# Kernel optimization log

Hardware: AMD Instinct MI355X
Metric: run time of the kernel (lower is better)

The kernel has to match this reference:

```python
import jax, jax.numpy as jnp
import numpy as np

B, NCOL, NCOND = 1024, 64, 64
NRODT, D, NEST, NFOREST, NHID, NCLASS = 1024, 4, 128, 100, 128, 10
EPS = 1e-5


def setup_inputs() -> dict:
    key = jax.random.key(0)
    ks = jax.random.split(key, 16)
    rng = np.random.default_rng(0)
    s = 0.1
    inp = {
        'x': jax.random.normal(ks[0], (B, NCOL), jnp.float32),
        # phi_1 numerical grouped conv: groups=NCOL, in_per_g=1, out_per_g=NCOND
        'w1': jax.random.normal(ks[1], (NCOL, 1, NCOND), jnp.float32) * s,
        'b1': jax.random.normal(ks[2], (NCOL * NCOND,), jnp.float32) * s,
        # rODTConstruction fixed permutation of the 4096 conditions
        'perm': jnp.asarray(rng.permutation(NCOND * NCOL), jnp.int32),
        'gn1_g': jnp.ones((NCOND * NCOL,), jnp.float32),
        'gn1_b': jnp.zeros((NCOND * NCOL,), jnp.float32),
        # phi_2 grouped convs: groups=NRODT, block D->D then D->1
        'w2a': jax.random.normal(ks[3], (NRODT, D, D), jnp.float32) * s,
        'b2a': jax.random.normal(ks[4], (NRODT * D,), jnp.float32) * s,
        'gn2_g': jnp.ones((NCOND * NCOL,), jnp.float32),
        'gn2_b': jnp.zeros((NCOND * NCOL,), jnp.float32),
        'w2b': jax.random.normal(ks[5], (NRODT, D, 1), jnp.float32) * s,
        'b2b': jax.random.normal(ks[6], (NRODT,), jnp.float32) * s,
        'E': jax.random.normal(ks[7], (NRODT, NHID), jnp.float32) * s,
        # eval-mode sample_without_replacement buffer: per-forest subset of rODTs
        'swr': jnp.asarray(np.argsort(rng.random((NFOREST, NRODT)), axis=-1)[:, :NEST], jnp.int32),
        'ln1_g': jnp.ones((NHID,), jnp.float32),
        'ln1_b': jnp.zeros((NHID,), jnp.float32),
        'lin1_w': jax.random.normal(ks[8], (NHID, NHID), jnp.float32) * s,
        'lin1_b': jax.random.normal(ks[9], (NHID,), jnp.float32) * s,
        'ln2_g': jnp.ones((NHID,), jnp.float32),
        'ln2_b': jnp.zeros((NHID,), jnp.float32),
        'lin2_w': jax.random.normal(ks[10], (NHID, NCLASS), jnp.float32) * s,
        'lin2_b': jax.random.normal(ks[11], (NCLASS,), jnp.float32) * s,
    }
    return inp


def _group_norm(v, g, gamma, beta):
    # v: (B, C), normalize within each of g channel groups (L=1 in the torch module)
    b, c = v.shape
    vg = v.reshape(b, g, c // g)
    mu = vg.mean(-1, keepdims=True)
    var = vg.var(-1, keepdims=True)
    vn = ((vg - mu) / jnp.sqrt(var + EPS)).reshape(b, c)
    return vn * gamma + beta


def _layer_norm(v, gamma, beta):
    mu = v.mean(-1, keepdims=True)
    var = v.var(-1, keepdims=True)
    return (v - mu) / jnp.sqrt(var + EPS) * gamma + beta


def reference(x, w1, b1, perm, gn1_g, gn1_b, w2a, b2a, gn2_g, gn2_b, w2b, b2b,
              E, swr, ln1_g, ln1_b, lin1_w, lin1_b, ln2_g, ln2_b, lin2_w, lin2_b):
    b = x.shape[0]
    # ConditionGeneration (numerical only): block-diag GEMV with in_per_group=1
    M = jax.nn.sigmoid(x[:, :, None] * w1[None, :, 0, :] + b1.reshape(NCOL, NCOND))  # (B, NCOL, NCOND)
    M = M.transpose(0, 2, 1)  # (B, NCOND, NCOL)
    # rODTConstruction: flatten + fixed permutation
    O = M.reshape(b, NCOND * NCOL)[:, perm]  # (B, 4096)
    # phi_2: GroupNorm -> grouped conv (D->D) -> ReLU -> GroupNorm -> grouped conv (D->1)
    h = _group_norm(O, NRODT, gn1_g, gn1_b).reshape(b, NRODT, D)
    h = jnp.einsum('bgi,gio->bgo', h, w2a) + b2a.reshape(NRODT, D)
    h = jax.nn.relu(h).reshape(b, NRODT * D)
    h = _group_norm(h, NRODT, gn2_g, gn2_b).reshape(b, NRODT, D)
    w = jnp.einsum('bgi,gio->bgo', h, w2b)[..., 0] + b2b  # (B, NRODT), n_head=1
    # forest construction: gather rODT subsets, softmax over estimators, weighted embed sum
    ws = jax.nn.softmax(w[:, swr], axis=-1)  # (B, NFOREST, NEST)
    Es = E[swr]  # (NFOREST, NEST, NHID)
    F = jnp.einsum('bfe,feh->bfh', ws, Es)  # (B, NFOREST, NHID)
    # phi_3 bagging MLP (eval mode: dropout = identity)
    z = _layer_norm(F, ln1_g, ln1_b)
    z = jax.nn.relu(z @ lin1_w + lin1_b)
    z = _layer_norm(z, ln2_g, ln2_b)
    y_hats = z @ lin2_w + lin2_b  # (B, NFOREST, NCLASS)
    return y_hats.mean(1)  # (B, NCLASS)
```

## Files before the change

### kernel.cpp

```cpp
#include <hip/hip_runtime.h>


#define B_      1024
#define NCOL_   64
#define NCOND_  64
#define NRODT_  1024
#define NEST_   128
#define NFOREST_ 100
#define NHID_   128
#define NCLASS_ 10
#define EPS_    1e-5f

typedef __bf16 bf16_t;
typedef bf16_t bf16x8 __attribute__((ext_vector_type(8)));
typedef float  f32x4  __attribute__((ext_vector_type(4)));

#define MFMA16(a,b,c) __builtin_amdgcn_mfma_f32_16x16x32_bf16(a,b,c,0,0,0)

#define EG_FRAGS   (NFOREST_*4*8*64)
#define W1_FRAGS   (4*8*64)
#define L2_FRAGS   (4*64)

__global__ __launch_bounds__(256) void k_prep(
    const float* __restrict__ E,     const int*   __restrict__ swr,
    const float* __restrict__ lin1w, const float* __restrict__ lin2w,
    const float* __restrict__ x,
    bf16_t* __restrict__ Eh,  bf16_t* __restrict__ El,
    bf16_t* __restrict__ Wh,  bf16_t* __restrict__ Wl,
    bf16_t* __restrict__ L2h, bf16_t* __restrict__ L2l,
    float*  __restrict__ x_t, float* __restrict__ accz)
{
    int blk = blockIdx.x, tid = threadIdx.x;
    if (blk < 800) {
        int t = blk * 256 + tid;
        int lane = t & 63, nn = (t >> 6) & 7, kk = (t >> 9) & 3, f = t >> 11;
        int q = lane >> 4, n = nn * 16 + (lane & 15);
        bf16x8 hi, lo;
#pragma unroll
        for (int j = 0; j < 8; ++j) {
            int e = kk * 32 + q * 8 + j;
            int r = swr[f * NEST_ + e];
            float v = E[r * NHID_ + n];
            bf16_t h = (bf16_t)v;
            hi[j] = h; lo[j] = (bf16_t)(v - (float)h);
        }
        *(bf16x8*)(Eh + (size_t)t * 8) = hi;
        *(bf16x8*)(El + (size_t)t * 8) = lo;
    } else if (blk < 808) {
        int t = (blk - 800) * 256 + tid;
        int lane = t & 63, nn = (t >> 6) & 7, kk = t >> 9;
        int q = lane >> 4, n = nn * 16 + (lane & 15);
        bf16x8 hi, lo;
#pragma unroll
        for (int j = 0; j < 8; ++j) {
            int k = kk * 32 + q * 8 + j;
            float v = lin1w[k * NHID_ + n];
            bf16_t h = (bf16_t)v;
            hi[j] = h; lo[j] = (bf16_t)(v - (float)h);
        }
        *(bf16x8*)(Wh + t * 8) = hi;
        *(bf16x8*)(Wl + t * 8) = lo;
    } else if (blk == 808) {
        int t = tid;
        int lane = t & 63, kk = t >> 6;
        int q = lane >> 4, n = lane & 15;
        bf16x8 hi, lo;
#pragma unroll
        for (int j = 0; j < 8; ++j) {
            int k = kk * 32 + q * 8 + j;
            float v = (n < NCLASS_) ? lin2w[k * NCLASS_ + n] : 0.f;
            bf16_t h = (bf16_t)v;
            hi[j] = h; lo[j] = (bf16_t)(v - (float)h);
        }
        *(bf16x8*)(L2h + t * 8) = hi;
        *(bf16x8*)(L2l + t * 8) = lo;
    } else if (blk < 1065) {
        int t = (blk - 809) * 256 + tid;
        x_t[t] = x[(t & 1023) * NCOL_ + (t >> 10)];
    } else {
        int t = (blk - 1065) * 256 + tid;
        if (t < B_ * NCLASS_) accz[t] = 0.f;
    }
}

__global__ __launch_bounds__(256) void k_rodt(
    const float* __restrict__ x_t,  const float* __restrict__ w1,
    const float* __restrict__ b1,   const int*  __restrict__ perm,
    const float* __restrict__ gn1g, const float* __restrict__ gn1b,
    const float* __restrict__ w2a,  const float* __restrict__ b2a,
    const float* __restrict__ gn2g, const float* __restrict__ gn2b,
    const float* __restrict__ w2b,  const float* __restrict__ b2b,
    float* __restrict__ w_t)
{
    int g  = blockIdx.x;
    int bq = threadIdx.x * 4;

    int4 p4 = ((const int4*)perm)[g];
    int col[4]  = { p4.x & 63, p4.y & 63, p4.z & 63, p4.w & 63 };
    int cond[4] = { p4.x >> 6, p4.y >> 6, p4.z >> 6, p4.w >> 6 };
    float w1v[4], b1v[4];
#pragma unroll
    for (int j = 0; j < 4; ++j) {
        w1v[j] = w1[col[j] * NCOND_ + cond[j]];
        b1v[j] = b1[col[j] * NCOND_ + cond[j]];
    }
    float4 g1  = ((const float4*)gn1g)[g];
    float4 o1  = ((const float4*)gn1b)[g];
    float4 ba  = ((const float4*)b2a)[g];
    float4 g2  = ((const float4*)gn2g)[g];
    float4 o2  = ((const float4*)gn2b)[g];
    float4 wb4 = ((const float4*)w2b)[g];
    float  bb  = b2b[g];
    float4 wa[4];
    const float4* w2a4 = (const float4*)w2a;
#pragma unroll
    for (int i = 0; i < 4; ++i) wa[i] = w2a4[g * 4 + i];

    float xv[4][4];
#pragma unroll
    for (int j = 0; j < 4; ++j) {
        float4 t = *(const float4*)&x_t[col[j] * B_ + bq];
        xv[j][0] = t.x; xv[j][1] = t.y; xv[j][2] = t.z; xv[j][3] = t.w;
    }

    float outv[4];
#pragma unroll
    for (int bi = 0; bi < 4; ++bi) {
        float v[4];
#pragma unroll
        for (int j = 0; j < 4; ++j) {
            float t = xv[j][bi] * w1v[j] + b1v[j];
            v[j] = 1.0f / (1.0f + __expf(-t));
        }
        float mu = (v[0] + v[1] + v[2] + v[3]) * 0.25f;
        float var = 0.f;
#pragma unroll
        for (int j = 0; j < 4; ++j) { float d = v[j] - mu; var += d * d; }
        var *= 0.25f;
        float rs = rsqrtf(var + EPS_);
        float h[4];
        h[0] = (v[0] - mu) * rs * g1.x + o1.x;
        h[1] = (v[1] - mu) * rs * g1.y + o1.y;
        h[2] = (v[2] - mu) * rs * g1.z + o1.z;
        h[3] = (v[3] - mu) * rs * g1.w + o1.w;

        float4 a = ba;
#pragma unroll
        for (int i = 0; i < 4; ++i) {
            a.x += h[i] * wa[i].x; a.y += h[i] * wa[i].y;
            a.z += h[i] * wa[i].z; a.w += h[i] * wa[i].w;
        }
        float t2[4];
        t2[0] = fmaxf(a.x, 0.f); t2[1] = fmaxf(a.y, 0.f);
        t2[2] = fmaxf(a.z, 0.f); t2[3] = fmaxf(a.w, 0.f);

        float mu2 = (t2[0] + t2[1] + t2[2] + t2[3]) * 0.25f;
        float var2 = 0.f;
#pragma unroll
        for (int j = 0; j < 4; ++j) { float d = t2[j] - mu2; var2 += d * d; }
        var2 *= 0.25f;
        float rs2 = rsqrtf(var2 + EPS_);

        float wvv = bb;
        wvv += ((t2[0] - mu2) * rs2 * g2.x + o2.x) * wb4.x;
        wvv += ((t2[1] - mu2) * rs2 * g2.y + o2.y) * wb4.y;
        wvv += ((t2[2] - mu2) * rs2 * g2.z + o2.z) * wb4.z;
        wvv += ((t2[3] - mu2) * rs2 * g2.w + o2.w) * wb4.w;
        outv[bi] = wvv;
    }
    *(float4*)&w_t[(size_t)g * B_ + bq] = make_float4(outv[0], outv[1], outv[2], outv[3]);
}

__global__ __launch_bounds__(256, 4) void k_forest(
    const float*  __restrict__ w_t, const int* __restrict__ swr,
    const bf16_t* __restrict__ Eh,  const bf16_t* __restrict__ El,
    const bf16_t* __restrict__ Wh,  const bf16_t* __restrict__ Wl,
    const bf16_t* __restrict__ L2h, const bf16_t* __restrict__ L2l,
    const float* __restrict__ ln1g, const float* __restrict__ ln1b,
    const float* __restrict__ lin1b,
    const float* __restrict__ ln2g, const float* __restrict__ ln2b,
    float* __restrict__ acc)
{
    __shared__ float zsh[4][16 * 132];

    int tid  = threadIdx.x;
    int wid  = tid >> 6;
    int lane = tid & 63;
    int q    = lane >> 4;
    int mc   = lane & 15;

    int n    = blockIdx.x;
    int swiz = (n & 7) * 200 + (n >> 3);
    int f    = swiz >> 4;
    int bt   = swiz & 15;
    int b0   = bt * 64 + wid * 16;

    const int* swrf = swr + f * NEST_;
    float* zw = zsh[wid];

    float ex[4][8];
    float mx = -1e30f;
#pragma unroll
    for (int kk = 0; kk < 4; ++kk) {
        int4 r0 = *(const int4*)(swrf + kk * 32 + q * 8);
        int4 r1 = *(const int4*)(swrf + kk * 32 + q * 8 + 4);
        int rr[8] = { r0.x, r0.y, r0.z, r0.w, r1.x, r1.y, r1.z, r1.w };
#pragma unroll
        for (int j = 0; j < 8; ++j) {
            float v = w_t[rr[j] * B_ + b0 + mc];
            ex[kk][j] = v;
            mx = fmaxf(mx, v);
        }
    }
    mx = fmaxf(mx, __shfl_xor(mx, 16));
    mx = fmaxf(mx, __shfl_xor(mx, 32));
    float s = 0.f;
#pragma unroll
    for (int kk = 0; kk < 4; ++kk)
#pragma unroll
        for (int j = 0; j < 8; ++j) { ex[kk][j] = __expf(ex[kk][j] - mx); s += ex[kk][j]; }
    s += __shfl_xor(s, 16);
    s += __shfl_xor(s, 32);
    float inv = 1.f / s;

    bf16x8 afr[4];
#pragma unroll
    for (int kk = 0; kk < 4; ++kk)
#pragma unroll
        for (int j = 0; j < 8; ++j) afr[kk][j] = (bf16_t)(ex[kk][j] * inv);

    f32x4 accF[8];
#pragma unroll
    for (int nn = 0; nn < 8; ++nn) accF[nn] = (f32x4){0.f, 0.f, 0.f, 0.f};
    const bf16x8* EHf = (const bf16x8*)Eh;
    const bf16x8* ELf = (const bf16x8*)El;
#pragma unroll
    for (int kk = 0; kk < 4; ++kk) {
        size_t bi = (size_t)(f * 4 + kk) * 8;
#pragma unroll
        for (int nn = 0; nn < 8; ++nn) {
            bf16x8 bh = EHf[(bi + nn) * 64 + lane];
            bf16x8 bl = ELf[(bi + nn) * 64 + lane];
            accF[nn] = MFMA16(afr[kk], bh, accF[nn]);
            accF[nn] = MFMA16(afr[kk], bl, accF[nn]);
        }
    }

    float mu[4], rs[4];
#pragma unroll
    for (int reg = 0; reg < 4; ++reg) {
        float ps = 0.f, pq = 0.f;
#pragma unroll
        for (int nn = 0; nn < 8; ++nn) { float v = accF[nn][reg]; ps += v; pq += v * v; }
#pragma unroll
        for (int o = 1; o <= 8; o <<= 1) { ps += __shfl_xor(ps, o); pq += __shfl_xor(pq, o); }
        float m_ = ps * (1.f / NHID_);
        mu[reg] = m_;
        rs[reg] = rsqrtf(pq * (1.f / NHID_) - m_ * m_ + EPS_);
    }
    {
#pragma unroll
        for (int nn = 0; nn < 8; ++nn) {
            int c = nn * 16 + mc;
            float gv = ln1g[c], bv = ln1b[c];
#pragma unroll
            for (int reg = 0; reg < 4; ++reg)
                zw[(q * 4 + reg) * 132 + c] = (accF[nn][reg] - mu[reg]) * rs[reg] * gv + bv;
        }
    }

    bf16x8 a2[4];
#pragma unroll
    for (int kk = 0; kk < 4; ++kk) {
        int dwb = kk * 32 + q * 8;
        f32x4 u0 = *(const f32x4*)&zw[mc * 132 + dwb];
        f32x4 u1 = *(const f32x4*)&zw[mc * 132 + dwb + 4];
#pragma unroll
        for (int j = 0; j < 4; ++j) { a2[kk][j] = (bf16_t)u0[j]; a2[kk][4 + j] = (bf16_t)u1[j]; }
    }
    f32x4 accA[8];
#pragma unroll
    for (int nn = 0; nn < 8; ++nn) accA[nn] = (f32x4){0.f, 0.f, 0.f, 0.f};
    const bf16x8* WHf = (const bf16x8*)Wh;
    const bf16x8* WLf = (const bf16x8*)Wl;
#pragma unroll
    for (int kk = 0; kk < 4; ++kk) {
#pragma unroll
        for (int nn = 0; nn < 8; ++nn) {
            bf16x8 bh = WHf[(kk * 8 + nn) * 64 + lane];
            bf16x8 bl = WLf[(kk * 8 + nn) * 64 + lane];
            accA[nn] = MFMA16(a2[kk], bh, accA[nn]);
            accA[nn] = MFMA16(a2[kk], bl, accA[nn]);
        }
    }

#pragma unroll
    for (int nn = 0; nn < 8; ++nn) {
        float bv = lin1b[nn * 16 + mc];
#pragma unroll
        for (int reg = 0; reg < 4; ++reg)
            accA[nn][reg] = fmaxf(accA[nn][reg] + bv, 0.f);
    }
    float mu2[4], rs2[4];
#pragma unroll
    for (int reg = 0; reg < 4; ++reg) {
        float ps = 0.f, pq = 0.f;
#pragma unroll
        for (int nn = 0; nn < 8; ++nn) { float v = accA[nn][reg]; ps += v; pq += v * v; }
#pragma unroll
        for (int o = 1; o <= 8; o <<= 1) { ps += __shfl_xor(ps, o); pq += __shfl_xor(pq, o); }
        float m_ = ps * (1.f / NHID_);
        mu2[reg] = m_;
        rs2[reg] = rsqrtf(pq * (1.f / NHID_) - m_ * m_ + EPS_);
    }
    {
#pragma unroll
        for (int nn = 0; nn < 8; ++nn) {
            int c = nn * 16 + mc;
            float gv = ln2g[c], bv = ln2b[c];
#pragma unroll
            for (int reg = 0; reg < 4; ++reg)
                zw[(q * 4 + reg) * 132 + c] = (accA[nn][reg] - mu2[reg]) * rs2[reg] * gv + bv;
        }
    }

    f32x4 accO = {0.f, 0.f, 0.f, 0.f};
    const bf16x8* LHf = (const bf16x8*)L2h;
    const bf16x8* LLf = (const bf16x8*)L2l;
#pragma unroll
    for (int kk = 0; kk < 4; ++kk) {
        int dwb = kk * 32 + q * 8;
        f32x4 u0 = *(const f32x4*)&zw[mc * 132 + dwb];
        f32x4 u1 = *(const f32x4*)&zw[mc * 132 + dwb + 4];
        bf16x8 a3;
#pragma unroll
        for (int j = 0; j < 4; ++j) { a3[j] = (bf16_t)u0[j]; a3[4 + j] = (bf16_t)u1[j]; }
        accO = MFMA16(a3, LHf[kk * 64 + lane], accO);
        accO = MFMA16(a3, LLf[kk * 64 + lane], accO);
    }
    if (mc < NCLASS_) {
#pragma unroll
        for (int reg = 0; reg < 4; ++reg)
            atomicAdd(&acc[(b0 + q * 4 + reg) * NCLASS_ + mc], accO[reg]);
    }
}

__global__ __launch_bounds__(256) void k_final(
    const float* __restrict__ acc, const float* __restrict__ lin2b,
    float* __restrict__ out)
{
    int i = blockIdx.x * 256 + threadIdx.x;
    if (i < B_ * NCLASS_) {
        int c = i % NCLASS_;
        out[i] = acc[i] * (1.f / NFOREST_) + lin2b[c];
    }
}

extern "C" void kernel_launch(void* const* d_in, const int* in_sizes, int n_in,
                              void* d_out, int out_size, void* d_ws, size_t ws_size,
                              hipStream_t stream)
{
    const float* x     = (const float*)d_in[0];
    const float* w1    = (const float*)d_in[1];
    const float* b1    = (const float*)d_in[2];
    const int*   perm  = (const int*)  d_in[3];
    const float* gn1g  = (const float*)d_in[4];
    const float* gn1b  = (const float*)d_in[5];
    const float* w2a   = (const float*)d_in[6];
    const float* b2a   = (const float*)d_in[7];
    const float* gn2g  = (const float*)d_in[8];
    const float* gn2b  = (const float*)d_in[9];
    const float* w2b   = (const float*)d_in[10];
    const float* b2b   = (const float*)d_in[11];
    const float* E     = (const float*)d_in[12];
    const int*   swr   = (const int*)  d_in[13];
    const float* ln1g  = (const float*)d_in[14];
    const float* ln1b  = (const float*)d_in[15];
    const float* lin1w = (const float*)d_in[16];
    const float* lin1b = (const float*)d_in[17];
    const float* ln2g  = (const float*)d_in[18];
    const float* ln2b  = (const float*)d_in[19];
    const float* lin2w = (const float*)d_in[20];
    const float* lin2b = (const float*)d_in[21];

    char* base = (char*)d_ws;
    float*  w_t  = (float*)base;
    float*  accp = (float*)(base + 4u * 1024 * 1024);
    float*  x_t  = (float*)(base + 4u * 1024 * 1024 + 64 * 1024);
    bf16_t* Eh   = (bf16_t*)(base + 4u * 1024 * 1024 + 64 * 1024 + 256 * 1024);
    bf16_t* El   = Eh  + (size_t)EG_FRAGS * 8;
    bf16_t* Wh   = El  + (size_t)EG_FRAGS * 8;
    bf16_t* Wl   = Wh  + (size_t)W1_FRAGS * 8;
    bf16_t* L2h  = Wl  + (size_t)W1_FRAGS * 8;
    bf16_t* L2l  = L2h + (size_t)L2_FRAGS * 8;

    k_prep<<<1105, 256, 0, stream>>>(E, swr, lin1w, lin2w, x,
                                     Eh, El, Wh, Wl, L2h, L2l, x_t, accp);

    k_rodt<<<NRODT_, 256, 0, stream>>>(
        x_t, w1, b1, perm, gn1g, gn1b, w2a, b2a, gn2g, gn2b, w2b, b2b, w_t);

    k_forest<<<NFOREST_ * 16, 256, 0, stream>>>(
        w_t, swr, Eh, El, Wh, Wl, L2h, L2l,
        ln1g, ln1b, lin1b, ln2g, ln2b, accp);

    k_final<<<(B_ * NCLASS_ + 255) / 256, 256, 0, stream>>>(
        accp, lin2b, (float*)d_out);
}
```

Baseline: 148.9 us.

## Split forest GEMM N-dimension across waves with shared-LDS A operands

Changes k_forest so each wave computes two N-tiles (32 columns) for all 64 rows of the block, instead of all 128 columns for its own 16 rows. A operands are staged in a shared bf16 LDS buffer and results are exchanged through an fp32 LDS buffer for the layer norms. Each wave now loads a quarter of the E/W1 weight fragments, cutting global/L2 traffic by 4x, at the cost of several __syncthreads, larger LDS use (about 51KB), and dropping the occupancy hint from launch bounds.

```diff
diff --git a/kernel.cpp b/kernel.cpp
--- a/kernel.cpp
+++ b/kernel.cpp
@@ -20,6 +20,8 @@
 #define EG_FRAGS   (NFOREST_*4*8*64)
 #define W1_FRAGS   (4*8*64)
 #define L2_FRAGS   (4*64)
+
+#define ZLD 136
 
 __global__ __launch_bounds__(256) void k_prep(
     const float* __restrict__ E,     const int*   __restrict__ swr,
@@ -171,7 +173,7 @@
     *(float4*)&w_t[(size_t)g * B_ + bq] = make_float4(outv[0], outv[1], outv[2], outv[3]);
 }
 
-__global__ __launch_bounds__(256, 4) void k_forest(
+__global__ __launch_bounds__(256) void k_forest(
     const float*  __restrict__ w_t, const int* __restrict__ swr,
     const bf16_t* __restrict__ Eh,  const bf16_t* __restrict__ El,
     const bf16_t* __restrict__ Wh,  const bf16_t* __restrict__ Wl,
@@ -181,7 +183,8 @@
     const float* __restrict__ ln2g, const float* __restrict__ ln2b,
     float* __restrict__ acc)
 {
-    __shared__ float zsh[4][16 * 132];
+    __shared__ __align__(16) float  zC[64 * 132];
+    __shared__ __align__(16) bf16_t zb[64 * ZLD];
 
     int tid  = threadIdx.x;
     int wid  = tid >> 6;
@@ -196,7 +199,7 @@
     int b0   = bt * 64 + wid * 16;
 
     const int* swrf = swr + f * NEST_;
-    float* zw = zsh[wid];
+    int nn0 = wid * 2;
 
     float ex[4][8];
     float mx = -1e30f;
@@ -223,104 +226,153 @@
     s += __shfl_xor(s, 32);
     float inv = 1.f / s;
 
-    bf16x8 afr[4];
-#pragma unroll
-    for (int kk = 0; kk < 4; ++kk)
-#pragma unroll
-        for (int j = 0; j < 8; ++j) afr[kk][j] = (bf16_t)(ex[kk][j] * inv);
-
-    f32x4 accF[8];
-#pragma unroll
-    for (int nn = 0; nn < 8; ++nn) accF[nn] = (f32x4){0.f, 0.f, 0.f, 0.f};
+#pragma unroll
+    for (int kk = 0; kk < 4; ++kk) {
+        bf16x8 v;
+#pragma unroll
+        for (int j = 0; j < 8; ++j) v[j] = (bf16_t)(ex[kk][j] * inv);
+        *(bf16x8*)&zb[(wid * 16 + mc) * ZLD + kk * 32 + q * 8] = v;
+    }
+
+    __syncthreads();
+
     const bf16x8* EHf = (const bf16x8*)Eh;
     const bf16x8* ELf = (const bf16x8*)El;
+    f32x4 accF[4][2];
+#pragma unroll
+    for (int mt = 0; mt < 4; ++mt) {
+        accF[mt][0] = (f32x4){0.f, 0.f, 0.f, 0.f};
+        accF[mt][1] = (f32x4){0.f, 0.f, 0.f, 0.f};
+    }
 #pragma unroll
     for (int kk = 0; kk < 4; ++kk) {
         size_t bi = (size_t)(f * 4 + kk) * 8;
-#pragma unroll
-        for (int nn = 0; nn < 8; ++nn) {
-            bf16x8 bh = EHf[(bi + nn) * 64 + lane];
-            bf16x8 bl = ELf[(bi + nn) * 64 + lane];
-            accF[nn] = MFMA16(afr[kk], bh, accF[nn]);
-            accF[nn] = MFMA16(afr[kk], bl, accF[nn]);
-        }
-    }
-
-    float mu[4], rs[4];
-#pragma unroll
-    for (int reg = 0; reg < 4; ++reg) {
-        float ps = 0.f, pq = 0.f;
-#pragma unroll
-        for (int nn = 0; nn < 8; ++nn) { float v = accF[nn][reg]; ps += v; pq += v * v; }
-#pragma unroll
-        for (int o = 1; o <= 8; o <<= 1) { ps += __shfl_xor(ps, o); pq += __shfl_xor(pq, o); }
-        float m_ = ps * (1.f / NHID_);
-        mu[reg] = m_;
-        rs[reg] = rsqrtf(pq * (1.f / NHID_) - m_ * m_ + EPS_);
-    }
+        bf16x8 bh0 = EHf[(bi + nn0) * 64 + lane];
+        bf16x8 bh1 = EHf[(bi + nn0 + 1) * 64 + lane];
+        bf16x8 bl0 = ELf[(bi + nn0) * 64 + lane];
+        bf16x8 bl1 = ELf[(bi + nn0 + 1) * 64 + lane];
+        bf16x8 av[4];
+#pragma unroll
+        for (int mt = 0; mt < 4; ++mt)
+            av[mt] = *(const bf16x8*)&zb[(mt * 16 + mc) * ZLD + kk * 32 + q * 8];
+#pragma unroll
+        for (int mt = 0; mt < 4; ++mt) {
+            accF[mt][0] = MFMA16(av[mt], bh0, accF[mt][0]);
+            accF[mt][1] = MFMA16(av[mt], bh1, accF[mt][1]);
+            accF[mt][0] = MFMA16(av[mt], bl0, accF[mt][0]);
+            accF[mt][1] = MFMA16(av[mt], bl1, accF[mt][1]);
+        }
+    }
+#pragma unroll
+    for (int mt = 0; mt < 4; ++mt)
+#pragma unroll
+        for (int nj = 0; nj < 2; ++nj)
+#pragma unroll
+            for (int reg = 0; reg < 4; ++reg)
+                zC[(mt * 16 + q * 4 + reg) * 132 + (nn0 + nj) * 16 + mc] = accF[mt][nj][reg];
+
+    __syncthreads();
+
     {
+        float vv[8][4];
+#pragma unroll
+        for (int nn = 0; nn < 8; ++nn)
+#pragma unroll
+            for (int reg = 0; reg < 4; ++reg)
+                vv[nn][reg] = zC[(wid * 16 + q * 4 + reg) * 132 + nn * 16 + mc];
+        float mu[4], rs[4];
+#pragma unroll
+        for (int reg = 0; reg < 4; ++reg) {
+            float ps = 0.f, pq = 0.f;
+#pragma unroll
+            for (int nn = 0; nn < 8; ++nn) { float v = vv[nn][reg]; ps += v; pq += v * v; }
+#pragma unroll
+            for (int o = 1; o <= 8; o <<= 1) { ps += __shfl_xor(ps, o); pq += __shfl_xor(pq, o); }
+            float m_ = ps * (1.f / NHID_);
+            mu[reg] = m_;
+            rs[reg] = rsqrtf(pq * (1.f / NHID_) - m_ * m_ + EPS_);
+        }
 #pragma unroll
         for (int nn = 0; nn < 8; ++nn) {
             int c = nn * 16 + mc;
             float gv = ln1g[c], bv = ln1b[c];
 #pragma unroll
             for (int reg = 0; reg < 4; ++reg)
-                zw[(q * 4 + reg) * 132 + c] = (accF[nn][reg] - mu[reg]) * rs[reg] * gv + bv;
-        }
-    }
-
-    bf16x8 a2[4];
-#pragma unroll
-    for (int kk = 0; kk < 4; ++kk) {
-        int dwb = kk * 32 + q * 8;
-        f32x4 u0 = *(const f32x4*)&zw[mc * 132 + dwb];
-        f32x4 u1 = *(const f32x4*)&zw[mc * 132 + dwb + 4];
-#pragma unroll
-        for (int j = 0; j < 4; ++j) { a2[kk][j] = (bf16_t)u0[j]; a2[kk][4 + j] = (bf16_t)u1[j]; }
-    }
-    f32x4 accA[8];
-#pragma unroll
-    for (int nn = 0; nn < 8; ++nn) accA[nn] = (f32x4){0.f, 0.f, 0.f, 0.f};
+                zb[(wid * 16 + q * 4 + reg) * ZLD + c] =
+                    (bf16_t)((vv[nn][reg] - mu[reg]) * rs[reg] * gv + bv);
+        }
+    }
+
+    __syncthreads();
+
     const bf16x8* WHf = (const bf16x8*)Wh;
     const bf16x8* WLf = (const bf16x8*)Wl;
+    f32x4 accA[4][2];
+#pragma unroll
+    for (int mt = 0; mt < 4; ++mt) {
+        accA[mt][0] = (f32x4){0.f, 0.f, 0.f, 0.f};
+        accA[mt][1] = (f32x4){0.f, 0.f, 0.f, 0.f};
+    }
 #pragma unroll
     for (int kk = 0; kk < 4; ++kk) {
+        bf16x8 bh0 = WHf[(kk * 8 + nn0) * 64 + lane];
+        bf16x8 bh1 = WHf[(kk * 8 + nn0 + 1) * 64 + lane];
+        bf16x8 bl0 = WLf[(kk * 8 + nn0) * 64 + lane];
+        bf16x8 bl1 = WLf[(kk * 8 + nn0 + 1) * 64 + lane];
+        bf16x8 av[4];
+#pragma unroll
+        for (int mt = 0; mt < 4; ++mt)
+            av[mt] = *(const bf16x8*)&zb[(mt * 16 + mc) * ZLD + kk * 32 + q * 8];
+#pragma unroll
+        for (int mt = 0; mt < 4; ++mt) {
+            accA[mt][0] = MFMA16(av[mt], bh0, accA[mt][0]);
+            accA[mt][1] = MFMA16(av[mt], bh1, accA[mt][1]);
+            accA[mt][0] = MFMA16(av[mt], bl0, accA[mt][0]);
+            accA[mt][1] = MFMA16(av[mt], bl1, accA[mt][1]);
+        }
+    }
+
+    __syncthreads();
+#pragma unroll
+    for (int mt = 0; mt < 4; ++mt)
+#pragma unroll
+        for (int nj = 0; nj < 2; ++nj)
+#pragma unroll
+            for (int reg = 0; reg < 4; ++reg)
+                zC[(mt * 16 + q * 4 + reg) * 132 + (nn0 + nj) * 16 + mc] = accA[mt][nj][reg];
+
+    __syncthreads();
+
+    {
+        float vv[8][4];
 #pragma unroll
         for (int nn = 0; nn < 8; ++nn) {
-            bf16x8 bh = WHf[(kk * 8 + nn) * 64 + lane];
-            bf16x8 bl = WLf[(kk * 8 + nn) * 64 + lane];
-            accA[nn] = MFMA16(a2[kk], bh, accA[nn]);
-            accA[nn] = MFMA16(a2[kk], bl, accA[nn]);
-        }
-    }
-
-#pragma unroll
-    for (int nn = 0; nn < 8; ++nn) {
-        float bv = lin1b[nn * 16 + mc];
-#pragma unroll
-        for (int reg = 0; reg < 4; ++reg)
-            accA[nn][reg] = fmaxf(accA[nn][reg] + bv, 0.f);
-    }
-    float mu2[4], rs2[4];
-#pragma unroll
-    for (int reg = 0; reg < 4; ++reg) {
-        float ps = 0.f, pq = 0.f;
-#pragma unroll
-        for (int nn = 0; nn < 8; ++nn) { float v = accA[nn][reg]; ps += v; pq += v * v; }
-#pragma unroll
-        for (int o = 1; o <= 8; o <<= 1) { ps += __shfl_xor(ps, o); pq += __shfl_xor(pq, o); }
-        float m_ = ps * (1.f / NHID_);
-        mu2[reg] = m_;
-        rs2[reg] = rsqrtf(pq * (1.f / NHID_) - m_ * m_ + EPS_);
-    }
-    {
+            float bv = lin1b[nn * 16 + mc];
+#pragma unroll
+            for (int reg = 0; reg < 4; ++reg)
+                vv[nn][reg] = fmaxf(
+                    zC[(wid * 16 + q * 4 + reg) * 132 + nn * 16 + mc] + bv, 0.f);
+        }
+        float mu2[4], rs2[4];
+#pragma unroll
+        for (int reg = 0; reg < 4; ++reg) {
+            float ps = 0.f, pq = 0.f;
+#pragma unroll
+            for (int nn = 0; nn < 8; ++nn) { float v = vv[nn][reg]; ps += v; pq += v * v; }
+#pragma unroll
+            for (int o = 1; o <= 8; o <<= 1) { ps += __shfl_xor(ps, o); pq += __shfl_xor(pq, o); }
+            float m_ = ps * (1.f / NHID_);
+            mu2[reg] = m_;
+            rs2[reg] = rsqrtf(pq * (1.f / NHID_) - m_ * m_ + EPS_);
+        }
 #pragma unroll
         for (int nn = 0; nn < 8; ++nn) {
             int c = nn * 16 + mc;
             float gv = ln2g[c], bv = ln2b[c];
 #pragma unroll
             for (int reg = 0; reg < 4; ++reg)
-                zw[(q * 4 + reg) * 132 + c] = (accA[nn][reg] - mu2[reg]) * rs2[reg] * gv + bv;
+                zb[(wid * 16 + q * 4 + reg) * ZLD + c] =
+                    (bf16_t)((vv[nn][reg] - mu2[reg]) * rs2[reg] * gv + bv);
         }
     }
 
@@ -329,12 +381,7 @@
     const bf16x8* LLf = (const bf16x8*)L2l;
 #pragma unroll
     for (int kk = 0; kk < 4; ++kk) {
-        int dwb = kk * 32 + q * 8;
-        f32x4 u0 = *(const f32x4*)&zw[mc * 132 + dwb];
-        f32x4 u1 = *(const f32x4*)&zw[mc * 132 + dwb + 4];
-        bf16x8 a3;
-#pragma unroll
-        for (int j = 0; j < 4; ++j) { a3[j] = (bf16_t)u0[j]; a3[4 + j] = (bf16_t)u1[j]; }
+        bf16x8 a3 = *(const bf16x8*)&zb[(wid * 16 + mc) * ZLD + kk * 32 + q * 8];
         accO = MFMA16(a3, LHf[kk * 64 + lane], accO);
         accO = MFMA16(a3, LLf[kk * 64 + lane], accO);
     }
```

Result: faster. 141.6 us (-4.9%).
